# Performance work log

Hardware: AMD Instinct MI355X
Metric: run time of the kernel (lower is better)

The kernel has to match this reference:

```python
import jax, jax.numpy as jnp
import numpy as np

VOCAB, HIDDEN, LAYERS = 128, 1024, 2
B, T = 128, 512


def setup_inputs() -> dict:
    key = jax.random.key(0)
    ks = jax.random.split(key, 8)
    s0 = 1.0 / np.sqrt(HIDDEN)
    x = jax.random.normal(ks[0], (B, T, VOCAB), dtype=jnp.float32)
    h = jnp.zeros((LAYERS, B, HIDDEN), dtype=jnp.float32)
    c = jnp.zeros((LAYERS, B, HIDDEN), dtype=jnp.float32)
    # LSTM params, gate order (i, f, g, o) concatenated along last dim (4H)
    Wx0 = jax.random.uniform(ks[1], (VOCAB, 4 * HIDDEN), jnp.float32, -s0, s0)
    Wh0 = jax.random.uniform(ks[2], (HIDDEN, 4 * HIDDEN), jnp.float32, -s0, s0)
    b0 = jax.random.uniform(ks[3], (4 * HIDDEN,), jnp.float32, -s0, s0)
    Wx1 = jax.random.uniform(ks[4], (HIDDEN, 4 * HIDDEN), jnp.float32, -s0, s0)
    Wh1 = jax.random.uniform(ks[5], (HIDDEN, 4 * HIDDEN), jnp.float32, -s0, s0)
    b1 = jax.random.uniform(ks[6], (4 * HIDDEN,), jnp.float32, -s0, s0)
    return {"x": x, "h": h, "c": c, "Wx0": Wx0, "Wh0": Wh0, "b0": b0,
            "Wx1": Wx1, "Wh1": Wh1, "b1": b1}


def _lstm_cell(inp, h_prev, c_prev, Wx, Wh, b):
    gates = inp @ Wx + h_prev @ Wh + b            # (B, 4H)
    i, f, g, o = jnp.split(gates, 4, axis=-1)
    i = jax.nn.sigmoid(i)
    f = jax.nn.sigmoid(f)
    g = jnp.tanh(g)
    o = jax.nn.sigmoid(o)
    c_new = f * c_prev + i * g
    h_new = o * jnp.tanh(c_new)
    return h_new, c_new


def reference(x, h, c, Wx0, Wh0, b0, Wx1, Wh1, b1):
    layer_params = [(Wx0, Wh0, b0), (Wx1, Wh1, b1)]

    def step(carry, x_t):
        h_prev, c_prev = carry                    # each (L, B, H)
        inp = x_t                                 # (B, VOCAB)
        hs, cs = [], []
        for l, (Wx, Wh, b) in enumerate(layer_params):
            h_new, c_new = _lstm_cell(inp, h_prev[l], c_prev[l], Wx, Wh, b)
            hs.append(h_new)
            cs.append(c_new)
            inp = h_new
        return (jnp.stack(hs), jnp.stack(cs)), hs[-1]

    xs = jnp.swapaxes(x, 0, 1)                    # (T, B, VOCAB)
    (h_f, c_f), outs = jax.lax.scan(step, (h, c), xs)
    outs = jnp.swapaxes(outs, 0, 1)               # (B, T, H)
    return outs, h_f, c_f
```

## Files before the change

kernel.cpp:

```cpp
#include <hip/hip_runtime.h>

#define VV 128
#define HH 1024
#define BB 128
#define TT 512
#define G4 4096
#define BTH ((size_t)BB * TT * HH)
#define HPAR (4 * 64 * 512)

typedef __attribute__((ext_vector_type(8))) short bf16x8;
typedef __attribute__((ext_vector_type(16))) float f32x16;

__device__ __forceinline__ short f2bf(float f) {
  unsigned u = __float_as_uint(f);
  u = (u + 0x7fffu + ((u >> 16) & 1u)) >> 16;
  return (short)u;
}

__device__ __forceinline__ float fsig(float x) {
  x = fminf(fmaxf(x, -30.f), 30.f);
  float e = __expf(-x);
  return 1.f / (1.f + e);
}
__device__ __forceinline__ float ftanh(float x) {
  x = fminf(fmaxf(x, -15.f), 15.f);
  float e = __expf(-2.f * x);
  return (1.f - e) / (1.f + e);
}


__global__ void conv_x(const float* __restrict__ x, short* __restrict__ xp) {
  const int n = TT * 4 * 8 * 512;
  for (int i = blockIdx.x * blockDim.x + threadIdx.x; i < n; i += gridDim.x * blockDim.x) {
    int e = i & 7, lane = (i >> 3) & 63, kc = (i >> 9) & 7, rb = (i >> 12) & 3, t = i >> 14;
    int row = rb * 32 + (lane & 31);
    int v = kc * 16 + ((lane >> 5) << 3) + e;
    xp[i] = f2bf(x[((size_t)row * TT + t) * VV + v]);
  }
}

__global__ void init_state(const float* __restrict__ h,
                           short* __restrict__ h0p, short* __restrict__ h1p) {
  const int n = 2 * HPAR;
  for (int i = blockIdx.x * blockDim.x + threadIdx.x; i < n; i += gridDim.x * blockDim.x) {
    int inner = i & (HPAR - 1);
    int l = i >> 17;
    int e = i & 7, lane = (i >> 3) & 63, kc = (i >> 9) & 63, rb = (i >> 15) & 3;
    int row = rb * 32 + (lane & 31);
    int j = kc * 16 + ((lane >> 5) << 3) + e;
    short hb = f2bf(h[((size_t)l * BB + row) * HH + j]);
    (l ? h1p : h0p)[HPAR + inner] = hb;
  }
}

__global__ void pack_w(const float* __restrict__ Wx0, const float* __restrict__ Wh0,
                       const float* __restrict__ Wx1, const float* __restrict__ Wh1,
                       short* __restrict__ wp0, short* __restrict__ wp1) {
  const int n0 = 128 * 72 * 512;
  const int n1 = 128 * 128 * 512;
  for (int i = blockIdx.x * blockDim.x + threadIdx.x; i < n0 + n1; i += gridDim.x * blockDim.x) {
    if (i < n0) {
      int cu = i / (72 * 512);
      int rem = i - cu * (72 * 512);
      int kc = rem >> 9, le = rem & 511;
      int lane = le >> 3, e = le & 7;
      int k = kc * 16 + ((lane >> 5) << 3) + e;
      int cl = lane & 31;
      int gcol = (cl >> 3) * HH + cu * 8 + (cl & 7);
      float f = (k < VV) ? Wx0[(size_t)k * G4 + gcol] : Wh0[(size_t)(k - VV) * G4 + gcol];
      wp0[i] = f2bf(f);
    } else {
      int j = i - n0;
      int cu = j >> 16;
      int rem = j & 65535;
      int kc = rem >> 9, le = rem & 511;
      int lane = le >> 3, e = le & 7;
      int k = kc * 16 + ((lane >> 5) << 3) + e;
      int cl = lane & 31;
      int gcol = (cl >> 3) * HH + cu * 8 + (cl & 7);
      float f = (k < HH) ? Wx1[(size_t)k * G4 + gcol] : Wh1[(size_t)(k - HH) * G4 + gcol];
      wp1[j] = f2bf(f);
    }
  }
}

__global__ void pack_b(const float* __restrict__ b0, const float* __restrict__ b1,
                       float* __restrict__ bp, unsigned* __restrict__ slots) {
  int i = blockIdx.x * blockDim.x + threadIdx.x;
  if (i < 2 * 128 * 32) {
    int l = i >> 12;
    int cu = (i >> 5) & 127;
    int cc = i & 31;
    const float* b = l ? b1 : b0;
    bp[i] = b[(cc >> 3) * HH + cu * 8 + (cc & 7)];
  }
  if (i < 256) slots[i] = 0u;
}


template <int NK>
__device__ __forceinline__ void gemm_plain(f32x16* acc, const short* __restrict__ pa,
                                           const short* __restrict__ pb) {
  #pragma unroll
  for (int kc = 0; kc < NK; ++kc) {
    bf16x8 a = *(const bf16x8*)(pa + kc * 512);
    bf16x8 b = *(const bf16x8*)(pb + kc * 512);
    acc[kc & 3] = __builtin_amdgcn_mfma_f32_32x32x16_bf16(a, b, acc[kc & 3], 0, 0, 0);
  }
}

__device__ __forceinline__ void gemm64_coh(f32x16* acc, const short* pa,
                                           const short* __restrict__ pb) {
  bf16x8 A0[16], A1[16];
  #pragma unroll
  for (int j = 0; j < 16; ++j)
    asm volatile("global_load_dwordx4 %0, %1, off sc0 sc1"
                 : "=v"(A0[j]) : "v"(pa + j * 512));
  #pragma unroll
  for (int c = 0; c < 4; ++c) {
    bf16x8* CUR = (c & 1) ? A1 : A0;
    bf16x8* NXT = (c & 1) ? A0 : A1;
    if (c < 3) {
      #pragma unroll
      for (int j = 0; j < 16; ++j)
        asm volatile("global_load_dwordx4 %0, %1, off sc0 sc1"
                     : "=v"(NXT[j]) : "v"(pa + (c + 1) * 16 * 512 + j * 512));
      asm volatile("s_waitcnt vmcnt(16)" ::: "memory");
    } else {
      asm volatile("s_waitcnt vmcnt(0)" ::: "memory");
    }
    #pragma unroll
    for (int j = 0; j < 16; ++j)
      asm volatile("" : "+v"(CUR[j]));
    #pragma unroll
    for (int j = 0; j < 16; ++j) {
      bf16x8 b = *(const bf16x8*)(pb + (c * 16 + j) * 512);
      acc[j & 3] = __builtin_amdgcn_mfma_f32_32x32x16_bf16(CUR[j], b, acc[j & 3], 0, 0, 0);
    }
  }
}

__global__ void __launch_bounds__(256, 1) lstm_main(const short* __restrict__ xp,
    short* __restrict__ h0p, short* __restrict__ h1p,
    const short* __restrict__ wp0, const short* __restrict__ wp1,
    const float* __restrict__ bpack, const float* __restrict__ cin,
    float* __restrict__ out, unsigned* __restrict__ slots) {
  __shared__ short wlds[128 * 512];
  const int blk = blockIdx.x;
  const int layer = blk >> 7;
  const int cu = blk & 127;
  const int tid = threadIdx.x;
  const int lane = tid & 63;
  const int wave = tid >> 6;

  const int nkc = layer ? 128 : 72;
  const short* wsrc = layer ? (wp1 + (size_t)cu * 128 * 512) : (wp0 + (size_t)cu * 72 * 512);
  for (int i = tid; i < nkc * 64; i += 256)
    ((int4*)wlds)[i] = ((const int4*)wsrc)[i];
  __syncthreads();

  const int col = lane & 31;
  const float bias = bpack[layer * 4096 + cu * 32 + col];
  const int uu = col & 7;
  const bool ewlane = (col < 8);
  const int gcol = cu * 8 + uu;
  const int hi4 = ((lane >> 5) << 2);

  float creg[16];
  #pragma unroll
  for (int r = 0; r < 16; ++r) {
    int grow = wave * 32 + (r & 3) + ((r >> 2) << 3) + hi4;
    creg[r] = ewlane ? cin[(size_t)layer * BB * HH + (size_t)grow * HH + gcol] : 0.f;
  }

  const int pst = (wave * 64 + (cu >> 1)) * 512 + ((cu & 1) << 8);

  for (int p = 0; p <= TT; ++p) {
    const bool active = layer ? (p >= 1) : (p < TT);
    if (active) {
      const int t = layer ? (p - 1) : p;
      f32x16 acc[4];
      #pragma unroll
      for (int r = 0; r < 16; ++r) {
        acc[0][r] = bias; acc[1][r] = 0.f; acc[2][r] = 0.f; acc[3][r] = 0.f;
      }
      const int parR = (p + 1) & 1;
      if (layer == 0) {
        gemm_plain<8>(acc, xp + ((size_t)(t * 4 + wave) * 8) * 512 + lane * 8,
                      wlds + lane * 8);
        gemm64_coh(acc, h0p + ((size_t)(parR * 4 + wave) * 64) * 512 + lane * 8,
                   wlds + 8 * 512 + lane * 8);
      } else {
        gemm64_coh(acc, h0p + ((size_t)(parR * 4 + wave) * 64) * 512 + lane * 8,
                   wlds + lane * 8);
        gemm64_coh(acc, h1p + ((size_t)(((p & 1)) * 4 + wave) * 64) * 512 + lane * 8,
                   wlds + 64 * 512 + lane * 8);
      }
      f32x16 accf = (acc[0] + acc[1]) + (acc[2] + acc[3]);
      short* hp = layer ? (h1p + (size_t)((p + 1) & 1) * HPAR)
                        : (h0p + (size_t)(p & 1) * HPAR);
      #pragma unroll
      for (int r = 0; r < 16; ++r) {
        float a0 = accf[r];
        float f_ = __shfl_xor(a0, 8);
        float g_ = __shfl_xor(a0, 16);
        float o_ = __shfl_xor(a0, 24);
        const int rloc = (r & 3) + ((r >> 2) << 3) + hi4;
        const int grow = wave * 32 + rloc;
        float hnew = 0.f;
        if (ewlane) {
          float iv = fsig(a0), fv = fsig(f_), gv = ftanh(g_), ov = fsig(o_);
          float cnew = fv * creg[r] + iv * gv;
          creg[r] = cnew;
          hnew = ov * ftanh(cnew);
        }
        unsigned hb = (unsigned short)f2bf(hnew);
        unsigned pb2 = (unsigned)__shfl_xor((int)hb, 1);
        if (ewlane) {
          if (layer) out[(size_t)grow * TT * HH + (size_t)t * HH + gcol] = hnew;
          if (t == TT - 1) {
            out[BTH + (size_t)layer * BB * HH + (size_t)grow * HH + gcol] = hnew;
            out[BTH + (size_t)(2 + layer) * BB * HH + (size_t)grow * HH + gcol] = creg[r];
          }
          if (!(uu & 1)) {
            unsigned dw = hb | (pb2 << 16);
            __hip_atomic_store((unsigned*)(hp + pst + rloc * 8 + uu), dw,
                               __ATOMIC_RELAXED, __HIP_MEMORY_SCOPE_AGENT);
          }
        }
      }
    }
    if (p == TT) break;

    __syncthreads();
    if (tid < 64) {
      if (tid == 0)
        __hip_atomic_store(&slots[blk], (unsigned)(p + 1),
                           __ATOMIC_RELAXED, __HIP_MEMORY_SCOPE_AGENT);
      const unsigned tgt = (unsigned)(p + 1);
      for (;;) {
        bool ok = true;
        #pragma unroll
        for (int j = 0; j < 4; ++j) {
          unsigned v = __hip_atomic_load(&slots[(tid << 2) + j],
                                         __ATOMIC_RELAXED, __HIP_MEMORY_SCOPE_AGENT);
          ok &= (v >= tgt);
        }
        if (__all(ok)) break;
        __builtin_amdgcn_s_sleep(2);
      }
      __atomic_signal_fence(__ATOMIC_SEQ_CST);
    }
    __syncthreads();
  }
}


extern "C" void kernel_launch(void* const* d_in, const int* in_sizes, int n_in,
                              void* d_out, int out_size, void* d_ws, size_t ws_size,
                              hipStream_t stream) {
  const float* x   = (const float*)d_in[0];
  const float* h   = (const float*)d_in[1];
  const float* c   = (const float*)d_in[2];
  const float* Wx0 = (const float*)d_in[3];
  const float* Wh0 = (const float*)d_in[4];
  const float* b0  = (const float*)d_in[5];
  const float* Wx1 = (const float*)d_in[6];
  const float* Wh1 = (const float*)d_in[7];
  const float* b1  = (const float*)d_in[8];
  float* out = (float*)d_out;

  char* ws = (char*)d_ws;
  short* xp  = (short*)ws;
  short* h0p = (short*)(ws + 16777216);
  short* h1p = (short*)(ws + 17301504);
  short* wp0 = (short*)(ws + 17825792);
  short* wp1 = (short*)(ws + 27262976);
  float* bp  = (float*)(ws + 44040192);
  unsigned* slots = (unsigned*)(ws + 44072960);

  hipLaunchKernelGGL(conv_x,     dim3(2048), dim3(256), 0, stream, x, xp);
  hipLaunchKernelGGL(init_state, dim3(512),  dim3(256), 0, stream, h, h0p, h1p);
  hipLaunchKernelGGL(pack_w,     dim3(4096), dim3(256), 0, stream, Wx0, Wh0, Wx1, Wh1, wp0, wp1);
  hipLaunchKernelGGL(pack_b,     dim3(32),   dim3(256), 0, stream, b0, b1, bp, slots);

  hipLaunchKernelGGL(lstm_main, dim3(256), dim3(256), 0, stream,
                     xp, h0p, h1p, wp0, wp1, bp, c, out, slots);
}
```

Baseline: 7.809 ms.

## Use hierarchical grid barrier and overlap x-GEMM and output stores with barrier wait

Replaces the flat all-block spin barrier with a two-level scheme: one block per group of 32 polls its group's slots and publishes a group flag, then every block polls only the 8 group flags. After a block signals arrival, it precomputes the next step's input-projection GEMM (layer 0) or writes the sequence output (layer 1) before waiting, so that work sits inside the barrier latency. The recurrent GEMM is merged into one triple-buffered loader covering both h0 and h1 for layer 1. Gate nonlinearities are computed once per lane before shuffling, so each lane evaluates one sigmoid or tanh instead of four. The two-level barrier adds an extra hop of latency, and the deeper A buffer increases register pressure.

```diff
diff --git a/kernel.cpp b/kernel.cpp
--- a/kernel.cpp
+++ b/kernel.cpp
@@ -94,49 +94,58 @@
     const float* b = l ? b1 : b0;
     bp[i] = b[(cc >> 3) * HH + cu * 8 + (cc & 7)];
   }
-  if (i < 256) slots[i] = 0u;
-}
-
-
-template <int NK>
-__device__ __forceinline__ void gemm_plain(f32x16* acc, const short* __restrict__ pa,
-                                           const short* __restrict__ pb) {
-  #pragma unroll
-  for (int kc = 0; kc < NK; ++kc) {
-    bf16x8 a = *(const bf16x8*)(pa + kc * 512);
-    bf16x8 b = *(const bf16x8*)(pb + kc * 512);
-    acc[kc & 3] = __builtin_amdgcn_mfma_f32_32x32x16_bf16(a, b, acc[kc & 3], 0, 0, 0);
-  }
-}
-
-__device__ __forceinline__ void gemm64_coh(f32x16* acc, const short* pa,
-                                           const short* __restrict__ pb) {
-  bf16x8 A0[16], A1[16];
-  #pragma unroll
-  for (int j = 0; j < 16; ++j)
-    asm volatile("global_load_dwordx4 %0, %1, off sc0 sc1"
-                 : "=v"(A0[j]) : "v"(pa + j * 512));
-  #pragma unroll
-  for (int c = 0; c < 4; ++c) {
-    bf16x8* CUR = (c & 1) ? A1 : A0;
-    bf16x8* NXT = (c & 1) ? A0 : A1;
-    if (c < 3) {
-      #pragma unroll
-      for (int j = 0; j < 16; ++j)
+  if (i < 512) slots[i] = 0u;
+}
+
+
+template <int NCH>
+__device__ __forceinline__ void hgemm(f32x16* acc, const short* pa0, const short* pa1,
+                                      const short* __restrict__ pb) {
+  constexpr int NG = NCH / 16;
+  bf16x8 A[3][16];
+#pragma unroll
+  for (int g = 0; g < 3; ++g) {
+#pragma unroll
+    for (int j = 0; j < 16; ++j) {
+      const int c = g * 16 + j;
+      const short* ap = (c < 64) ? (pa0 + c * 512) : (pa1 + (c - 64) * 512);
+      asm volatile("global_load_dwordx4 %0, %1, off sc0 sc1" : "=v"(A[g][j]) : "v"(ap));
+    }
+  }
+#pragma unroll
+  for (int g = 0; g < NG; ++g) {
+    const int rem = NG - 1 - g;
+    if (rem >= 2)      asm volatile("s_waitcnt vmcnt(32)" ::: "memory");
+    else if (rem == 1) asm volatile("s_waitcnt vmcnt(16)" ::: "memory");
+    else               asm volatile("s_waitcnt vmcnt(0)" ::: "memory");
+#pragma unroll
+    for (int j = 0; j < 16; ++j)
+      asm volatile("" : "+v"(A[g % 3][j]));
+#pragma unroll
+    for (int j = 0; j < 16; ++j) {
+      const int c = g * 16 + j;
+      bf16x8 b = *(const bf16x8*)(pb + c * 512);
+      acc[j & 3] = __builtin_amdgcn_mfma_f32_32x32x16_bf16(A[g % 3][j], b, acc[j & 3], 0, 0, 0);
+    }
+    if (g + 3 < NG) {
+#pragma unroll
+      for (int j = 0; j < 16; ++j) {
+        const int c = (g + 3) * 16 + j;
+        const short* ap = (c < 64) ? (pa0 + c * 512) : (pa1 + (c - 64) * 512);
         asm volatile("global_load_dwordx4 %0, %1, off sc0 sc1"
-                     : "=v"(NXT[j]) : "v"(pa + (c + 1) * 16 * 512 + j * 512));
-      asm volatile("s_waitcnt vmcnt(16)" ::: "memory");
-    } else {
-      asm volatile("s_waitcnt vmcnt(0)" ::: "memory");
-    }
-    #pragma unroll
-    for (int j = 0; j < 16; ++j)
-      asm volatile("" : "+v"(CUR[j]));
-    #pragma unroll
-    for (int j = 0; j < 16; ++j) {
-      bf16x8 b = *(const bf16x8*)(pb + (c * 16 + j) * 512);
-      acc[j & 3] = __builtin_amdgcn_mfma_f32_32x32x16_bf16(CUR[j], b, acc[j & 3], 0, 0, 0);
-    }
+                     : "=v"(A[(g + 3) % 3][j]) : "v"(ap));
+      }
+    }
+  }
+}
+
+__device__ __forceinline__ void xgemm(f32x16* acc, const short* __restrict__ pax,
+                                      const short* __restrict__ pb) {
+#pragma unroll
+  for (int c = 0; c < 8; ++c) {
+    bf16x8 a = *(const bf16x8*)(pax + c * 512);
+    bf16x8 b = *(const bf16x8*)(pb + c * 512);
+    acc[c & 3] = __builtin_amdgcn_mfma_f32_32x32x16_bf16(a, b, acc[c & 3], 0, 0, 0);
   }
 }
 
@@ -146,6 +155,7 @@
     const float* __restrict__ bpack, const float* __restrict__ cin,
     float* __restrict__ out, unsigned* __restrict__ slots) {
   __shared__ short wlds[128 * 512];
+  unsigned* gdone = slots + 256;
   const int blk = blockIdx.x;
   const int layer = blk >> 7;
   const int cu = blk & 127;
@@ -166,58 +176,89 @@
   const int gcol = cu * 8 + uu;
   const int hi4 = ((lane >> 5) << 2);
 
-  float creg[16];
-  #pragma unroll
+  float creg[16], hval[16];
+#pragma unroll
   for (int r = 0; r < 16; ++r) {
     int grow = wave * 32 + (r & 3) + ((r >> 2) << 3) + hi4;
     creg[r] = ewlane ? cin[(size_t)layer * BB * HH + (size_t)grow * HH + gcol] : 0.f;
+    hval[r] = 0.f;
   }
 
   const int pst = (wave * 64 + (cu >> 1)) * 512 + ((cu & 1) << 8);
 
+  f32x16 acc[4];
+  auto initacc = [&]() {
+#pragma unroll
+    for (int r = 0; r < 16; ++r) {
+      acc[0][r] = bias; acc[1][r] = 0.f; acc[2][r] = 0.f; acc[3][r] = 0.f;
+    }
+  };
+
+  if (layer == 0) {
+    initacc();
+    xgemm(acc, xp + ((size_t)(0 * 4 + wave) * 8) * 512 + lane * 8, wlds + lane * 8);
+  }
+
   for (int p = 0; p <= TT; ++p) {
+    if (p > 0) {
+      const unsigned tgt = (unsigned)p;
+      if ((blk & 31) == 0 && tid < 32) {
+        for (;;) {
+          unsigned v = __hip_atomic_load(&slots[blk + tid],
+                                         __ATOMIC_RELAXED, __HIP_MEMORY_SCOPE_AGENT);
+          if (__all(v >= tgt)) break;
+          __builtin_amdgcn_s_sleep(1);
+        }
+        if (tid == 0)
+          __hip_atomic_store(&gdone[(blk >> 5) << 5], tgt,
+                             __ATOMIC_RELAXED, __HIP_MEMORY_SCOPE_AGENT);
+      }
+      if (tid < 8) {
+        for (;;) {
+          unsigned v = __hip_atomic_load(&gdone[tid << 5],
+                                         __ATOMIC_RELAXED, __HIP_MEMORY_SCOPE_AGENT);
+          if (__all(v >= tgt)) break;
+          __builtin_amdgcn_s_sleep(1);
+        }
+      }
+      __syncthreads();
+    }
+
     const bool active = layer ? (p >= 1) : (p < TT);
+    const int t = layer ? (p - 1) : p;
     if (active) {
-      const int t = layer ? (p - 1) : p;
-      f32x16 acc[4];
-      #pragma unroll
-      for (int r = 0; r < 16; ++r) {
-        acc[0][r] = bias; acc[1][r] = 0.f; acc[2][r] = 0.f; acc[3][r] = 0.f;
-      }
       const int parR = (p + 1) & 1;
       if (layer == 0) {
-        gemm_plain<8>(acc, xp + ((size_t)(t * 4 + wave) * 8) * 512 + lane * 8,
-                      wlds + lane * 8);
-        gemm64_coh(acc, h0p + ((size_t)(parR * 4 + wave) * 64) * 512 + lane * 8,
-                   wlds + 8 * 512 + lane * 8);
+        hgemm<64>(acc, h0p + ((size_t)(parR * 4 + wave) * 64) * 512 + lane * 8,
+                  h0p, wlds + 8 * 512 + lane * 8);
       } else {
-        gemm64_coh(acc, h0p + ((size_t)(parR * 4 + wave) * 64) * 512 + lane * 8,
+        initacc();
+        hgemm<128>(acc, h0p + ((size_t)(parR * 4 + wave) * 64) * 512 + lane * 8,
+                   h1p + ((size_t)((p & 1) * 4 + wave) * 64) * 512 + lane * 8,
                    wlds + lane * 8);
-        gemm64_coh(acc, h1p + ((size_t)(((p & 1)) * 4 + wave) * 64) * 512 + lane * 8,
-                   wlds + 64 * 512 + lane * 8);
       }
       f32x16 accf = (acc[0] + acc[1]) + (acc[2] + acc[3]);
       short* hp = layer ? (h1p + (size_t)((p + 1) & 1) * HPAR)
                         : (h0p + (size_t)(p & 1) * HPAR);
-      #pragma unroll
+#pragma unroll
       for (int r = 0; r < 16; ++r) {
         float a0 = accf[r];
-        float f_ = __shfl_xor(a0, 8);
-        float g_ = __shfl_xor(a0, 16);
-        float o_ = __shfl_xor(a0, 24);
+        float nl = (col >= 16 && col < 24) ? ftanh(a0) : fsig(a0);
+        float f_ = __shfl_xor(nl, 8);
+        float g_ = __shfl_xor(nl, 16);
+        float o_ = __shfl_xor(nl, 24);
         const int rloc = (r & 3) + ((r >> 2) << 3) + hi4;
         const int grow = wave * 32 + rloc;
         float hnew = 0.f;
         if (ewlane) {
-          float iv = fsig(a0), fv = fsig(f_), gv = ftanh(g_), ov = fsig(o_);
-          float cnew = fv * creg[r] + iv * gv;
+          float cnew = f_ * creg[r] + nl * g_;
           creg[r] = cnew;
-          hnew = ov * ftanh(cnew);
+          hnew = o_ * ftanh(cnew);
+          hval[r] = hnew;
         }
         unsigned hb = (unsigned short)f2bf(hnew);
         unsigned pb2 = (unsigned)__shfl_xor((int)hb, 1);
         if (ewlane) {
-          if (layer) out[(size_t)grow * TT * HH + (size_t)t * HH + gcol] = hnew;
           if (t == TT - 1) {
             out[BTH + (size_t)layer * BB * HH + (size_t)grow * HH + gcol] = hnew;
             out[BTH + (size_t)(2 + layer) * BB * HH + (size_t)grow * HH + gcol] = creg[r];
@@ -230,28 +271,37 @@
         }
       }
     }
-    if (p == TT) break;
+
+    if (p == TT) {
+      if (layer && active && ewlane) {
+#pragma unroll
+        for (int r = 0; r < 16; ++r) {
+          const int rloc = (r & 3) + ((r >> 2) << 3) + hi4;
+          const int grow = wave * 32 + rloc;
+          out[(size_t)grow * TT * HH + (size_t)t * HH + gcol] = hval[r];
+        }
+      }
+      break;
+    }
 
     __syncthreads();
-    if (tid < 64) {
-      if (tid == 0)
-        __hip_atomic_store(&slots[blk], (unsigned)(p + 1),
-                           __ATOMIC_RELAXED, __HIP_MEMORY_SCOPE_AGENT);
-      const unsigned tgt = (unsigned)(p + 1);
-      for (;;) {
-        bool ok = true;
-        #pragma unroll
-        for (int j = 0; j < 4; ++j) {
-          unsigned v = __hip_atomic_load(&slots[(tid << 2) + j],
-                                         __ATOMIC_RELAXED, __HIP_MEMORY_SCOPE_AGENT);
-          ok &= (v >= tgt);
-        }
-        if (__all(ok)) break;
-        __builtin_amdgcn_s_sleep(2);
-      }
-      __atomic_signal_fence(__ATOMIC_SEQ_CST);
-    }
-    __syncthreads();
+    if (tid == 0)
+      __hip_atomic_store(&slots[blk], (unsigned)(p + 1),
+                         __ATOMIC_RELAXED, __HIP_MEMORY_SCOPE_AGENT);
+
+    if (layer == 0) {
+      if (p + 1 < TT) {
+        initacc();
+        xgemm(acc, xp + ((size_t)((p + 1) * 4 + wave) * 8) * 512 + lane * 8, wlds + lane * 8);
+      }
+    } else if (active && ewlane) {
+#pragma unroll
+      for (int r = 0; r < 16; ++r) {
+        const int rloc = (r & 3) + ((r >> 2) << 3) + hi4;
+        const int grow = wave * 32 + rloc;
+        out[(size_t)grow * TT * HH + (size_t)t * HH + gcol] = hval[r];
+      }
+    }
   }
 }
 
```

Result: faster. 6.390 ms (-18.2%).

## Replace grid barrier with per-slice flags and a ring of hidden-state buffers

Applied to the files above, without the earlier changes.

Drops the global all-block barrier at every step. Each wave now publishes a per-(layer, block, row-slice) step counter and consumers poll only the flags they need. Hidden states go into a 32-entry ring buffer so layer 0 can run ahead of layer 1, and blocks grow to 8 waves that split the K dimension in two and combine partial sums through LDS. The x conversion kernel is removed and x is converted to bf16 on the fly inside the GEMM. The risks are subtle memory-ordering bugs under relaxed atomics and extra LDS and register pressure.

```diff
diff --git a/kernel.cpp b/kernel.cpp
--- a/kernel.cpp
+++ b/kernel.cpp
@@ -7,9 +7,11 @@
 #define G4 4096
 #define BTH ((size_t)BB * TT * HH)
 #define HPAR (4 * 64 * 512)
+#define RING 32
 
 typedef __attribute__((ext_vector_type(8))) short bf16x8;
 typedef __attribute__((ext_vector_type(16))) float f32x16;
+typedef __attribute__((ext_vector_type(4))) unsigned u32x4;
 
 __device__ __forceinline__ short f2bf(float f) {
   unsigned u = __float_as_uint(f);
@@ -28,19 +30,13 @@
   return (1.f - e) / (1.f + e);
 }
 
-
-__global__ void conv_x(const float* __restrict__ x, short* __restrict__ xp) {
-  const int n = TT * 4 * 8 * 512;
-  for (int i = blockIdx.x * blockDim.x + threadIdx.x; i < n; i += gridDim.x * blockDim.x) {
-    int e = i & 7, lane = (i >> 3) & 63, kc = (i >> 9) & 7, rb = (i >> 12) & 3, t = i >> 14;
-    int row = rb * 32 + (lane & 31);
-    int v = kc * 16 + ((lane >> 5) << 3) + e;
-    xp[i] = f2bf(x[((size_t)row * TT + t) * VV + v]);
-  }
-}
+__device__ __forceinline__ unsigned eidx(int t) {
+  return ((unsigned)(t + 1) * 37u) & (RING - 1);
+}
+
 
 __global__ void init_state(const float* __restrict__ h,
-                           short* __restrict__ h0p, short* __restrict__ h1p) {
+                           short* __restrict__ h0dst, short* __restrict__ h1dst) {
   const int n = 2 * HPAR;
   for (int i = blockIdx.x * blockDim.x + threadIdx.x; i < n; i += gridDim.x * blockDim.x) {
     int inner = i & (HPAR - 1);
@@ -49,7 +45,7 @@
     int row = rb * 32 + (lane & 31);
     int j = kc * 16 + ((lane >> 5) << 3) + e;
     short hb = f2bf(h[((size_t)l * BB + row) * HH + j]);
-    (l ? h1p : h0p)[HPAR + inner] = hb;
+    (l ? h1dst : h0dst)[inner] = hb;
   }
 }
 
@@ -94,68 +90,92 @@
     const float* b = l ? b1 : b0;
     bp[i] = b[(cc >> 3) * HH + cu * 8 + (cc & 7)];
   }
-  if (i < 256) slots[i] = 0u;
-}
-
-
-template <int NK>
-__device__ __forceinline__ void gemm_plain(f32x16* acc, const short* __restrict__ pa,
-                                           const short* __restrict__ pb) {
-  #pragma unroll
-  for (int kc = 0; kc < NK; ++kc) {
-    bf16x8 a = *(const bf16x8*)(pa + kc * 512);
-    bf16x8 b = *(const bf16x8*)(pb + kc * 512);
-    acc[kc & 3] = __builtin_amdgcn_mfma_f32_32x32x16_bf16(a, b, acc[kc & 3], 0, 0, 0);
-  }
-}
-
-__device__ __forceinline__ void gemm64_coh(f32x16* acc, const short* pa,
-                                           const short* __restrict__ pb) {
-  bf16x8 A0[16], A1[16];
-  #pragma unroll
+  if (i < 2048) slots[i] = 0u;
+}
+
+
+__device__ __forceinline__ void pollge(const unsigned* s, unsigned tgt, int lane) {
+  const unsigned* p0 = s + (lane << 3);
+  for (;;) {
+    u32x4 a, b;
+    asm volatile("global_load_dwordx4 %0, %2, off sc0 sc1\n\t"
+                 "global_load_dwordx4 %1, %3, off sc0 sc1\n\t"
+                 "s_waitcnt vmcnt(0)"
+                 : "=v"(a), "=v"(b) : "v"(p0), "v"(p0 + 4) : "memory");
+    int ok = (a[0] >= tgt) & (a[1] >= tgt) & (a[2] >= tgt) & (a[3] >= tgt) &
+             (b[0] >= tgt) & (b[1] >= tgt) & (b[2] >= tgt) & (b[3] >= tgt);
+    if (__all(ok)) break;
+  }
+}
+
+template <int NG>
+__device__ __forceinline__ void hgemmN(f32x16* acc, const short* pa,
+                                       const short* __restrict__ pb) {
+  bf16x8 A[2][16];
+#pragma unroll
   for (int j = 0; j < 16; ++j)
-    asm volatile("global_load_dwordx4 %0, %1, off sc0 sc1"
-                 : "=v"(A0[j]) : "v"(pa + j * 512));
-  #pragma unroll
-  for (int c = 0; c < 4; ++c) {
-    bf16x8* CUR = (c & 1) ? A1 : A0;
-    bf16x8* NXT = (c & 1) ? A0 : A1;
-    if (c < 3) {
-      #pragma unroll
+    asm volatile("global_load_dwordx4 %0, %1, off sc0" : "=v"(A[0][j]) : "v"(pa + j * 512));
+#pragma unroll
+  for (int j = 0; j < 16; ++j)
+    asm volatile("global_load_dwordx4 %0, %1, off sc0" : "=v"(A[1][j]) : "v"(pa + (16 + j) * 512));
+#pragma unroll
+  for (int g = 0; g < NG; ++g) {
+    if (g + 1 < NG) asm volatile("s_waitcnt vmcnt(16)" ::: "memory");
+    else            asm volatile("s_waitcnt vmcnt(0)" ::: "memory");
+#pragma unroll
+    for (int j = 0; j < 16; ++j)
+      asm volatile("" : "+v"(A[g & 1][j]));
+#pragma unroll
+    for (int j = 0; j < 16; ++j) {
+      bf16x8 b = *(const bf16x8*)(pb + (g * 16 + j) * 512);
+      acc[j & 3] = __builtin_amdgcn_mfma_f32_32x32x16_bf16(A[g & 1][j], b, acc[j & 3], 0, 0, 0);
+    }
+    if (g + 2 < NG) {
+#pragma unroll
       for (int j = 0; j < 16; ++j)
-        asm volatile("global_load_dwordx4 %0, %1, off sc0 sc1"
-                     : "=v"(NXT[j]) : "v"(pa + (c + 1) * 16 * 512 + j * 512));
-      asm volatile("s_waitcnt vmcnt(16)" ::: "memory");
-    } else {
-      asm volatile("s_waitcnt vmcnt(0)" ::: "memory");
-    }
-    #pragma unroll
-    for (int j = 0; j < 16; ++j)
-      asm volatile("" : "+v"(CUR[j]));
-    #pragma unroll
-    for (int j = 0; j < 16; ++j) {
-      bf16x8 b = *(const bf16x8*)(pb + (c * 16 + j) * 512);
-      acc[j & 3] = __builtin_amdgcn_mfma_f32_32x32x16_bf16(CUR[j], b, acc[j & 3], 0, 0, 0);
-    }
-  }
-}
-
-__global__ void __launch_bounds__(256, 1) lstm_main(const short* __restrict__ xp,
-    short* __restrict__ h0p, short* __restrict__ h1p,
+        asm volatile("global_load_dwordx4 %0, %1, off sc0"
+                     : "=v"(A[g & 1][j]) : "v"(pa + ((g + 2) * 16 + j) * 512));
+    }
+  }
+}
+
+__device__ __forceinline__ void xgemm(f32x16* acc, const float* __restrict__ xlane,
+                                      const short* __restrict__ pb) {
+#pragma unroll
+  for (int c = 0; c < 8; ++c) {
+    float4 lo = *(const float4*)(xlane + c * 16);
+    float4 hi = *(const float4*)(xlane + c * 16 + 4);
+    bf16x8 a;
+    a[0] = f2bf(lo.x); a[1] = f2bf(lo.y); a[2] = f2bf(lo.z); a[3] = f2bf(lo.w);
+    a[4] = f2bf(hi.x); a[5] = f2bf(hi.y); a[6] = f2bf(hi.z); a[7] = f2bf(hi.w);
+    bf16x8 b = *(const bf16x8*)(pb + c * 512);
+    acc[c & 3] = __builtin_amdgcn_mfma_f32_32x32x16_bf16(a, b, acc[c & 3], 0, 0, 0);
+  }
+}
+
+
+__global__ void __launch_bounds__(512, 2) lstm_main(const float* __restrict__ x,
+    short* __restrict__ h0r, short* __restrict__ h1r,
     const short* __restrict__ wp0, const short* __restrict__ wp1,
     const float* __restrict__ bpack, const float* __restrict__ cin,
     float* __restrict__ out, unsigned* __restrict__ slots) {
   __shared__ short wlds[128 * 512];
+  __shared__ f32x16 aexch[4][64];
+  __shared__ short hstage[4][256];
+  unsigned* h0slots = slots;
+  unsigned* h1slots = slots + 512;
   const int blk = blockIdx.x;
   const int layer = blk >> 7;
   const int cu = blk & 127;
   const int tid = threadIdx.x;
   const int lane = tid & 63;
   const int wave = tid >> 6;
+  const int q = wave & 3;
+  const bool isB = wave >= 4;
 
   const int nkc = layer ? 128 : 72;
   const short* wsrc = layer ? (wp1 + (size_t)cu * 128 * 512) : (wp0 + (size_t)cu * 72 * 512);
-  for (int i = tid; i < nkc * 64; i += 256)
+  for (int i = tid; i < nkc * 64; i += 512)
     ((int4*)wlds)[i] = ((const int4*)wsrc)[i];
   __syncthreads();
 
@@ -164,94 +184,98 @@
   const int uu = col & 7;
   const bool ewlane = (col < 8);
   const int gcol = cu * 8 + uu;
-  const int hi4 = ((lane >> 5) << 2);
+  const int hi4 = (lane >> 5) << 2;
+  const int koff = (lane >> 5) << 3;
+  const size_t qsl = (size_t)q * 64 * 512 + lane * 8;
+  const float* xl = x + (size_t)(q * 32 + col) * (TT * VV) + koff;
 
   float creg[16];
-  #pragma unroll
-  for (int r = 0; r < 16; ++r) {
-    int grow = wave * 32 + (r & 3) + ((r >> 2) << 3) + hi4;
-    creg[r] = ewlane ? cin[(size_t)layer * BB * HH + (size_t)grow * HH + gcol] : 0.f;
-  }
-
-  const int pst = (wave * 64 + (cu >> 1)) * 512 + ((cu & 1) << 8);
+  if (!isB) {
+#pragma unroll
+    for (int r = 0; r < 16; ++r) {
+      int grow = q * 32 + (r & 3) + ((r >> 2) << 3) + hi4;
+      creg[r] = ewlane ? cin[(size_t)layer * BB * HH + (size_t)grow * HH + gcol] : 0.f;
+    }
+  }
 
   for (int p = 0; p <= TT; ++p) {
-    const bool active = layer ? (p >= 1) : (p < TT);
+    if (!layer && p == TT) break;
+    const bool active = layer ? (p >= 1) : true;
+    const int t = layer ? (p - 1) : p;
+    f32x16 accp;
     if (active) {
-      const int t = layer ? (p - 1) : p;
       f32x16 acc[4];
-      #pragma unroll
+#pragma unroll
       for (int r = 0; r < 16; ++r) {
-        acc[0][r] = bias; acc[1][r] = 0.f; acc[2][r] = 0.f; acc[3][r] = 0.f;
+        acc[0][r] = isB ? 0.f : bias; acc[1][r] = 0.f; acc[2][r] = 0.f; acc[3][r] = 0.f;
       }
-      const int parR = (p + 1) & 1;
-      if (layer == 0) {
-        gemm_plain<8>(acc, xp + ((size_t)(t * 4 + wave) * 8) * 512 + lane * 8,
-                      wlds + lane * 8);
-        gemm64_coh(acc, h0p + ((size_t)(parR * 4 + wave) * 64) * 512 + lane * 8,
-                   wlds + 8 * 512 + lane * 8);
+      if (!layer) {
+        const short* he = h0r + (size_t)eidx(p - 1) * HPAR + qsl;
+        if (!isB) {
+          if (p) pollge(h0slots, (unsigned)p, lane);
+          hgemmN<2>(acc, he, wlds + 8 * 512 + lane * 8);
+        } else {
+          xgemm(acc, xl + (size_t)t * VV, wlds + lane * 8);
+          if (p >= 25) pollge(h1slots, (unsigned)(p - 24), lane);
+          if (p) pollge(h0slots, (unsigned)p, lane);
+          hgemmN<2>(acc, he + 32 * 512, wlds + 40 * 512 + lane * 8);
+        }
       } else {
-        gemm64_coh(acc, h0p + ((size_t)(parR * 4 + wave) * 64) * 512 + lane * 8,
-                   wlds + lane * 8);
-        gemm64_coh(acc, h1p + ((size_t)(((p & 1)) * 4 + wave) * 64) * 512 + lane * 8,
-                   wlds + 64 * 512 + lane * 8);
+        if (!isB) {
+          pollge(h0slots, (unsigned)p, lane);
+          hgemmN<4>(acc, h0r + (size_t)eidx(p - 1) * HPAR + qsl, wlds + lane * 8);
+        } else {
+          pollge(h1slots, (unsigned)p, lane);
+          hgemmN<4>(acc, h1r + (size_t)eidx(p - 2) * HPAR + qsl, wlds + 64 * 512 + lane * 8);
+        }
       }
-      f32x16 accf = (acc[0] + acc[1]) + (acc[2] + acc[3]);
-      short* hp = layer ? (h1p + (size_t)((p + 1) & 1) * HPAR)
-                        : (h0p + (size_t)(p & 1) * HPAR);
-      #pragma unroll
-      for (int r = 0; r < 16; ++r) {
-        float a0 = accf[r];
-        float f_ = __shfl_xor(a0, 8);
-        float g_ = __shfl_xor(a0, 16);
-        float o_ = __shfl_xor(a0, 24);
-        const int rloc = (r & 3) + ((r >> 2) << 3) + hi4;
-        const int grow = wave * 32 + rloc;
-        float hnew = 0.f;
-        if (ewlane) {
-          float iv = fsig(a0), fv = fsig(f_), gv = ftanh(g_), ov = fsig(o_);
-          float cnew = fv * creg[r] + iv * gv;
-          creg[r] = cnew;
-          hnew = ov * ftanh(cnew);
-        }
-        unsigned hb = (unsigned short)f2bf(hnew);
-        unsigned pb2 = (unsigned)__shfl_xor((int)hb, 1);
-        if (ewlane) {
-          if (layer) out[(size_t)grow * TT * HH + (size_t)t * HH + gcol] = hnew;
-          if (t == TT - 1) {
-            out[BTH + (size_t)layer * BB * HH + (size_t)grow * HH + gcol] = hnew;
-            out[BTH + (size_t)(2 + layer) * BB * HH + (size_t)grow * HH + gcol] = creg[r];
-          }
-          if (!(uu & 1)) {
-            unsigned dw = hb | (pb2 << 16);
-            __hip_atomic_store((unsigned*)(hp + pst + rloc * 8 + uu), dw,
-                               __ATOMIC_RELAXED, __HIP_MEMORY_SCOPE_AGENT);
+      f32x16 s = (acc[0] + acc[1]) + (acc[2] + acc[3]);
+      if (isB) aexch[q][lane] = s;
+      else accp = s;
+    }
+    __syncthreads();
+    if (!isB) {
+      if (active) {
+        f32x16 accf = accp + aexch[q][lane];
+        short* hp = (layer ? h1r + (size_t)eidx(p - 1) * HPAR
+                           : h0r + (size_t)eidx(p) * HPAR)
+                    + ((size_t)q * 64 + (cu >> 1)) * 512 + ((cu & 1) << 8);
+#pragma unroll
+        for (int r = 0; r < 16; ++r) {
+          float a0 = accf[r];
+          float nl = (col >= 16 && col < 24) ? ftanh(a0) : fsig(a0);
+          float f_ = __shfl_xor(nl, 8);
+          float g_ = __shfl_xor(nl, 16);
+          float o_ = __shfl_xor(nl, 24);
+          const int rloc = (r & 3) + ((r >> 2) << 3) + hi4;
+          const int grow = q * 32 + rloc;
+          if (ewlane) {
+            float cnew = f_ * creg[r] + nl * g_;
+            creg[r] = cnew;
+            float hnew = o_ * ftanh(cnew);
+            hstage[q][rloc * 8 + uu] = f2bf(hnew);
+            if (layer) out[(size_t)grow * TT * HH + (size_t)t * HH + gcol] = hnew;
+            if (t == TT - 1) {
+              out[BTH + (size_t)layer * BB * HH + (size_t)grow * HH + gcol] = hnew;
+              out[BTH + (size_t)(2 + layer) * BB * HH + (size_t)grow * HH + gcol] = cnew;
+            }
           }
         }
+        if (lane < 32) {
+          bf16x8 v = *(const bf16x8*)&hstage[q][lane * 8];
+          asm volatile("global_store_dwordx4 %0, %1, off sc0 sc1"
+                       :: "v"(hp + lane * 8), "v"(v) : "memory");
+        }
+        asm volatile("s_waitcnt vmcnt(0)" ::: "memory");
+        if (lane == 0)
+          __hip_atomic_store(&slots[(layer << 9) + (cu << 2) + q], (unsigned)(p + 1),
+                             __ATOMIC_RELAXED, __HIP_MEMORY_SCOPE_AGENT);
+      } else if (layer && p == 0) {
+        if (lane == 0)
+          __hip_atomic_store(&h1slots[(cu << 2) + q], 1u,
+                             __ATOMIC_RELAXED, __HIP_MEMORY_SCOPE_AGENT);
       }
     }
-    if (p == TT) break;
-
-    __syncthreads();
-    if (tid < 64) {
-      if (tid == 0)
-        __hip_atomic_store(&slots[blk], (unsigned)(p + 1),
-                           __ATOMIC_RELAXED, __HIP_MEMORY_SCOPE_AGENT);
-      const unsigned tgt = (unsigned)(p + 1);
-      for (;;) {
-        bool ok = true;
-        #pragma unroll
-        for (int j = 0; j < 4; ++j) {
-          unsigned v = __hip_atomic_load(&slots[(tid << 2) + j],
-                                         __ATOMIC_RELAXED, __HIP_MEMORY_SCOPE_AGENT);
-          ok &= (v >= tgt);
-        }
-        if (__all(ok)) break;
-        __builtin_amdgcn_s_sleep(2);
-      }
-      __atomic_signal_fence(__ATOMIC_SEQ_CST);
-    }
-    __syncthreads();
   }
 }
 
@@ -271,19 +295,17 @@
   float* out = (float*)d_out;
 
   char* ws = (char*)d_ws;
-  short* xp  = (short*)ws;
-  short* h0p = (short*)(ws + 16777216);
-  short* h1p = (short*)(ws + 17301504);
-  short* wp0 = (short*)(ws + 17825792);
-  short* wp1 = (short*)(ws + 27262976);
-  float* bp  = (float*)(ws + 44040192);
-  unsigned* slots = (unsigned*)(ws + 44072960);
-
-  hipLaunchKernelGGL(conv_x,     dim3(2048), dim3(256), 0, stream, x, xp);
-  hipLaunchKernelGGL(init_state, dim3(512),  dim3(256), 0, stream, h, h0p, h1p);
+  short* wp0 = (short*)ws;
+  short* wp1 = (short*)(ws + 9437184);
+  float* bp  = (float*)(ws + 26214400);
+  unsigned* slots = (unsigned*)(ws + 26247168);
+  short* h0r = (short*)(ws + 26255360);
+  short* h1r = (short*)(ws + 34643968);
+
+  hipLaunchKernelGGL(init_state, dim3(512),  dim3(256), 0, stream, h, h0r, h1r);
   hipLaunchKernelGGL(pack_w,     dim3(4096), dim3(256), 0, stream, Wx0, Wh0, Wx1, Wh1, wp0, wp1);
   hipLaunchKernelGGL(pack_b,     dim3(32),   dim3(256), 0, stream, b0, b1, bp, slots);
 
-  hipLaunchKernelGGL(lstm_main, dim3(256), dim3(256), 0, stream,
-                     xp, h0p, h1p, wp0, wp1, bp, c, out, slots);
-}
+  hipLaunchKernelGGL(lstm_main, dim3(256), dim3(512), 0, stream,
+                     x, h0r, h1r, wp0, wp1, bp, c, out, slots);
+}
```

New measurement: 16.89 ms. +116.3%, slower.
